# Kernel tuning notes

Measured on AMD Instinct MI355X. Metric: run time of the kernel, lower is better.

The kernel has to match this reference:

```python
import jax, jax.numpy as jnp
import numpy as np

NN_SIZE = 16  # nn_size from __init__


def _knn_idx(points_ref, k):
    """Brute-force KNN of points_ref against itself (replaces faiss_knn).
    Returns (B, N, k) neighbor indices, self point excluded."""
    sq = jnp.sum(points_ref * points_ref, axis=-1)  # (B, N)
    # squared pairwise distances (B, N, N)
    d2 = sq[:, :, None] + sq[:, None, :] - 2.0 * jnp.einsum(
        'bnd,bmd->bnm', points_ref, points_ref)
    _, idx = jax.lax.top_k(-d2, k + 1)  # nearest first; idx[...,0] is self
    return idx[:, :, 1:]


def _edge_lengths(pts, knn_idx):
    """Gather neighbor coords and compute edge lengths (B, N, K)."""
    group = jax.vmap(lambda p, i: p[i])(pts, knn_idx)  # (B, N, K, D)
    return jnp.linalg.norm(group - pts[:, :, None, :], axis=-1)


def setup_inputs() -> dict:
    key = jax.random.key(0)
    k1, k2 = jax.random.split(key)
    B, N, D = 4, 8192, 3
    points_ref = jax.random.normal(k1, (B, N, D), dtype=jnp.float32)
    # pred points: perturbed ref so the loss is non-degenerate
    points = points_ref + 0.01 * jax.random.normal(k2, (B, N, D), dtype=jnp.float32)
    return {"points_ref": points_ref, "points": points}


def reference(points_ref, points):
    # faiss KNN is non-differentiable -> stop_gradient on the index search
    knn_idx = _knn_idx(jax.lax.stop_gradient(points_ref), NN_SIZE)  # (B,N,K)
    dist_ref = _edge_lengths(points_ref, knn_idx)  # (B, N, K)
    dist = _edge_lengths(points, knn_idx)          # (B, N, K)
    # metric = torch.nn.L1Loss() (mean reduction)
    return jnp.mean(jnp.abs(dist_ref - dist))
```

## Files before the change

kernel.cpp:

```cpp
#include <hip/hip_runtime.h>
#include <math.h>

#define BATCH 4
#define NPTS  8192
#define KNN   16
#define KK    17
#define NQ    (BATCH*NPTS)
#define JMASK 0x1FFFu
#define EMASK 0xFFFFE000u
#define TOTAL_EDGES (BATCH*NPTS*KNN)

#define GC    32
#define GLO   (-4.5f)
#define GINV  (32.0f/9.0f)
#define NCELL (GC*GC*GC)

#define NG    128
#define GSZ   64

#define QPB   16
#define BLOCK 256
#define GRIDQ (NQ/QPB)
#define WIN   64
#define CAP   21

__device__ __forceinline__ int cell_coord(float x) {
    int c = (int)floorf((x - GLO) * GINV);
    return min(GC - 1, max(0, c));
}
__device__ __forceinline__ unsigned spread5(unsigned v) {
    v &= 31u;
    v = (v | (v << 8)) & 0x100Fu;
    v = (v | (v << 4)) & 0x10C3u;
    v = (v | (v << 2)) & 0x1249u;
    return v;
}
__device__ __forceinline__ unsigned morton_id(float x, float y, float z) {
    return spread5((unsigned)cell_coord(x)) | (spread5((unsigned)cell_coord(y)) << 1)
         | (spread5((unsigned)cell_coord(z)) << 2);
}
__device__ __forceinline__ unsigned mkkey(const float4 p, float xi, float yi,
                                          float zi, float sqi, unsigned j) {
    const float e  = fmaf(p.x, xi, fmaf(p.y, yi, p.z * zi)) + p.w;
    const float d2 = e + sqi;
    return (__float_as_uint(d2) & EMASK) | j;
}
__device__ __forceinline__ void ins17(unsigned (&a)[KK], unsigned key) {
    #pragma unroll
    for (int k = KK - 1; k >= 1; --k) a[k] = min(a[k], max(a[k - 1], key));
    a[0] = min(a[0], key);
}
template<int RL>
__device__ __forceinline__ unsigned merge_tau(const unsigned (*s_key)[BLOCK], int t) {
    const int mq = t & (QPB - 1), half = (t >> 4) & 1;
    unsigned m[KK];
    #pragma unroll
    for (int k = 0; k < KK; ++k) m[k] = 0xFFFFFFFFu;
    for (int s = 8 * half; s < 8 * half + 8; ++s) {
        const int col = mq + s * QPB;
        for (int k = 0; k < RL; ++k) {
            const unsigned c = s_key[k][col];
            if (c >= m[KK - 1]) break;
            ins17(m, c);
        }
    }
    unsigned tau = 0;
    #pragma unroll
    for (int k = 0; k < KK; ++k) {
        const unsigned bk = (unsigned)__shfl_xor((int)m[KK - 1 - k], 16, 64);
        tau = max(tau, min(m[k], bk));
    }
    return tau;
}

__global__ void pel_hist(const float* __restrict__ pref, unsigned* __restrict__ hist,
                         float* __restrict__ acc, unsigned* __restrict__ bcnt) {
    const int idx = blockIdx.x * 256 + threadIdx.x;
    if (idx == 0) { acc[0] = 0.0f; bcnt[0] = 0u; }
    const int b = idx >> 13;
    const unsigned mid = morton_id(pref[3*idx], pref[3*idx+1], pref[3*idx+2]);
    atomicAdd(&hist[b * NCELL + mid], 1u);
}
__global__ __launch_bounds__(1024)
void pel_scan(const unsigned* __restrict__ hist, unsigned* __restrict__ off) {
    __shared__ unsigned s[1024];
    const unsigned* h = hist + blockIdx.x * NCELL;
    unsigned*       o = off  + blockIdx.x * NCELL;
    const int t = threadIdx.x;
    unsigned v[32], tot = 0;
    #pragma unroll
    for (int k = 0; k < 32; ++k) { v[k] = h[t * 32 + k]; tot += v[k]; }
    s[t] = tot;
    __syncthreads();
    for (int d = 1; d < 1024; d <<= 1) {
        const unsigned add = (t >= d) ? s[t - d] : 0u;
        __syncthreads();
        s[t] += add;
        __syncthreads();
    }
    unsigned run = s[t] - tot;
    #pragma unroll
    for (int k = 0; k < 32; ++k) { o[t * 32 + k] = run; run += v[k]; }
}
__global__ void pel_scatter(const float* __restrict__ pref, const float* __restrict__ pts,
                            unsigned* __restrict__ off,
                            float4* __restrict__ p4r, float4* __restrict__ p4p) {
    const int idx = blockIdx.x * 256 + threadIdx.x;
    const int b = idx >> 13;
    const float x = pref[3*idx], y = pref[3*idx+1], z = pref[3*idx+2];
    const unsigned mid = morton_id(x, y, z);
    const unsigned pos = atomicAdd(&off[b * NCELL + mid], 1u);
    p4r[b * NPTS + pos] = make_float4(-2.f*x, -2.f*y, -2.f*z, fmaf(x, x, fmaf(y, y, z*z)));
    const float px = pts[3*idx], py = pts[3*idx+1], pz = pts[3*idx+2];
    p4p[b * NPTS + pos] = make_float4(-2.f*px, -2.f*py, -2.f*pz,
                                      fmaf(px, px, fmaf(py, py, pz*pz)));
}
__global__ __launch_bounds__(256)
void pel_gstat(const float4* __restrict__ P4r, float4* __restrict__ gball) {
    const int wv = threadIdx.x >> 6, lane = threadIdx.x & 63;
    const int gid = blockIdx.x * 4 + wv;
    const int b = gid >> 7, g = gid & (NG - 1);
    const float4 p = P4r[b * NPTS + g * GSZ + lane];
    const float x = -0.5f * p.x, y = -0.5f * p.y, z = -0.5f * p.z;
    float mnx = x, mxx = x, mny = y, mxy = y, mnz = z, mxz = z;
    #pragma unroll
    for (int m = 1; m <= 32; m <<= 1) {
        mnx = fminf(mnx, __shfl_xor(mnx, m, 64)); mxx = fmaxf(mxx, __shfl_xor(mxx, m, 64));
        mny = fminf(mny, __shfl_xor(mny, m, 64)); mxy = fmaxf(mxy, __shfl_xor(mxy, m, 64));
        mnz = fminf(mnz, __shfl_xor(mnz, m, 64)); mxz = fmaxf(mxz, __shfl_xor(mxz, m, 64));
    }
    const float cx = 0.5f * (mnx + mxx), cy = 0.5f * (mny + mxy), cz = 0.5f * (mnz + mxz);
    float d = sqrtf((x-cx)*(x-cx) + (y-cy)*(y-cy) + (z-cz)*(z-cz));
    #pragma unroll
    for (int m = 1; m <= 32; m <<= 1) d = fmaxf(d, __shfl_xor(d, m, 64));
    if (lane == 0) gball[gid] = make_float4(cx, cy, cz, d);
}

__global__ __launch_bounds__(BLOCK, 8)
void pel_query(const float4* __restrict__ P4r, const float4* __restrict__ P4p,
               const float4* __restrict__ gball,
               float* __restrict__ acc_ws, unsigned* __restrict__ bcnt,
               float* __restrict__ out)
{
    __shared__ unsigned s_key[CAP][BLOCK];
    __shared__ unsigned s_tau[QPB];
    __shared__ unsigned short s_glist[NG];
    __shared__ float s_grp[4];
    __shared__ int s_ng;
    __shared__ float s_part[BLOCK / 64];

    const int t  = threadIdx.x;
    const int lq = t & (QPB - 1), sp = t >> 4;
    const int bid = blockIdx.x;
    const int qg  = ((bid & 7) << 8) | (bid >> 3);
    const int q  = qg * QPB + lq;
    const int b  = q >> 13;
    const int i  = q & (NPTS - 1);

    const float4* __restrict__ Pq = P4r + b * NPTS;
    const float4* __restrict__ Pp = P4p + b * NPTS;
    const float4* __restrict__ Gb = gball + b * NG;

    const float4 self = Pq[i];
    const float xi = -0.5f * self.x, yi = -0.5f * self.y, zi = -0.5f * self.z;
    const float sqi = self.w;

    unsigned al[4] = {~0u, ~0u, ~0u, ~0u};
    const int w0 = min(max(i - WIN / 2, 0), NPTS - WIN) + sp * 4;
    {
        float4 cw[4];
        #pragma unroll
        for (int u = 0; u < 4; ++u) cw[u] = Pq[w0 + u];
        #pragma unroll
        for (int u = 0; u < 4; ++u) {
            const unsigned key = mkkey(cw[u], xi, yi, zi, sqi, (unsigned)(w0 + u));
            #pragma unroll
            for (int k = 3; k >= 1; --k) al[k] = min(al[k], max(al[k - 1], key));
            al[0] = min(al[0], key);
        }
    }
    #pragma unroll
    for (int k = 0; k < 4; ++k) s_key[k][t] = al[k];
    __syncthreads();
    if (t < 32) {
        const unsigned tau0 = merge_tau<4>(s_key, t);
        if (t < QPB) s_tau[t] = tau0;
    }
    __syncthreads();

    if (t < QPB) {
        if (t == 0) s_ng = 0;
        const int i2 = (qg * QPB + t) & (NPTS - 1);
        const float4 s2 = Pq[i2];
        const float qx = -0.5f * s2.x, qy = -0.5f * s2.y, qz = -0.5f * s2.z;
        float mnx = qx, mxx = qx, mny = qy, mxy = qy, mnz = qz, mxz = qz;
        #pragma unroll
        for (int m = 1; m <= 8; m <<= 1) {
            mnx = fminf(mnx, __shfl_xor(mnx, m, 64)); mxx = fmaxf(mxx, __shfl_xor(mxx, m, 64));
            mny = fminf(mny, __shfl_xor(mny, m, 64)); mxy = fmaxf(mxy, __shfl_xor(mxy, m, 64));
            mnz = fminf(mnz, __shfl_xor(mnz, m, 64)); mxz = fmaxf(mxz, __shfl_xor(mxz, m, 64));
        }
        const float cx = 0.5f * (mnx + mxx), cy = 0.5f * (mny + mxy), cz = 0.5f * (mnz + mxz);
        const float dq = sqrtf((qx-cx)*(qx-cx) + (qy-cy)*(qy-cy) + (qz-cz)*(qz-cz));
        const float rt = sqrtf(__uint_as_float((s_tau[t] & EMASK) + 0x2000u));
        float v = dq + rt;
        #pragma unroll
        for (int m = 1; m <= 8; m <<= 1) v = fmaxf(v, __shfl_xor(v, m, 64));
        if (t == 0) {
            s_grp[0] = cx; s_grp[1] = cy; s_grp[2] = cz; s_grp[3] = v + 1e-3f;
        }
    }
    __syncthreads();

    if (t < NG) {
        const float4 gb = Gb[t];
        const float dx = gb.x - s_grp[0], dy = gb.y - s_grp[1], dz = gb.z - s_grp[2];
        const float rhs = s_grp[3] + gb.w;
        if (dx*dx + dy*dy + dz*dz <= rhs * rhs) {
            const int slot = atomicAdd(&s_ng, 1);
            s_glist[slot] = (unsigned short)t;
        }
    }
    __syncthreads();
    const int ng = s_ng;

    unsigned tauL = s_tau[lq];
    int cnt = 0;
    unsigned* skp = &s_key[0][t];
    int gb4n = (int)s_glist[0] * GSZ + sp * 4;
    float4 cn[4];
    #pragma unroll
    for (int u = 0; u < 4; ++u) cn[u] = Pq[gb4n + u];
    for (int gi = 0; gi < ng; ++gi) {
        const int gb4 = gb4n;
        float4 c[4];
        #pragma unroll
        for (int u = 0; u < 4; ++u) c[u] = cn[u];
        const int gin = (gi + 1 < ng) ? gi + 1 : gi;
        gb4n = (int)s_glist[gin] * GSZ + sp * 4;
        #pragma unroll
        for (int u = 0; u < 4; ++u) cn[u] = Pq[gb4n + u];

        #pragma unroll
        for (int u = 0; u < 4; ++u) {
            const unsigned key = mkkey(c[u], xi, yi, zi, sqi, (unsigned)(gb4 + u));
            *skp = key;
            const int a = (key <= tauL) ? 1 : 0;
            skp += a * BLOCK;
            cnt += a;
        }
        if (cnt > CAP - 4) {
            unsigned k17[KK];
            #pragma unroll
            for (int k = 0; k < KK; ++k) k17[k] = 0xFFFFFFFFu;
            for (int n = 0; n < cnt; ++n) ins17(k17, s_key[n][t]);
            const unsigned th = k17[KK - 1];
            int kept = 0;
            for (int n = 0; n < cnt; ++n) {
                const unsigned c2 = s_key[n][t];
                if (c2 <= th) { s_key[kept][t] = c2; ++kept; }
            }
            cnt = kept; tauL = min(tauL, th);
            skp = &s_key[cnt][t];
        }
    }

    unsigned c17[KK];
    #pragma unroll
    for (int k = 0; k < KK; ++k) c17[k] = 0xFFFFFFFFu;
    for (int n = 0; n < cnt; ++n) ins17(c17, s_key[n][t]);
    __syncthreads();
    #pragma unroll
    for (int k = 0; k < KK; ++k) s_key[k][t] = c17[k];
    __syncthreads();
    if (t < 32) {
        const unsigned tauX = merge_tau<KK>(s_key, t);
        if (t < QPB) s_tau[t] = tauX;
    }
    __syncthreads();
    const unsigned tauK = s_tau[lq];

    const float4 selfp = Pp[i];
    const float pxi = -0.5f * selfp.x, pyi = -0.5f * selfp.y, pzi = -0.5f * selfp.z;
    float accv = 0.0f;
    #pragma unroll
    for (int k = 0; k < KK; ++k) {
        if (c17[k] <= tauK) {
            const int j = (int)(c17[k] & JMASK);
            const float4 pr = Pq[j];
            const float er  = fmaf(pr.x, xi, fmaf(pr.y, yi, pr.z * zi)) + pr.w;
            const float d2r = fmaxf(er + sqi, 0.0f);
            const float4 pp = Pp[j];
            const float ep  = fmaf(pp.x, pxi, fmaf(pp.y, pyi, pp.z * pzi)) + pp.w;
            const float d2p = fmaxf(ep + selfp.w, 0.0f);
            accv += fabsf(sqrtf(d2r) - sqrtf(d2p));
        }
    }

    #pragma unroll
    for (int o = 32; o > 0; o >>= 1) accv += __shfl_down(accv, o, 64);
    if ((t & 63) == 0) s_part[t >> 6] = accv;
    __syncthreads();
    if (t == 0) {
        float s = 0.0f;
        #pragma unroll
        for (int w2 = 0; w2 < BLOCK / 64; ++w2) s += s_part[w2];
        atomicAdd(acc_ws, s);
        __threadfence();
        const unsigned old = atomicAdd(bcnt, 1u);
        if (old == GRIDQ - 1) {
            __threadfence();
            const float total = atomicAdd(acc_ws, 0.0f);
            out[0] = total * (1.0f / (float)TOTAL_EDGES);
        }
    }
}

extern "C" void kernel_launch(void* const* d_in, const int* in_sizes, int n_in,
                              void* d_out, int out_size, void* d_ws, size_t ws_size,
                              hipStream_t stream) {
    const float* pref = (const float*)d_in[0];
    const float* pts  = (const float*)d_in[1];
    float4*   P4r  = (float4*)d_ws;
    float4*   P4p  = P4r + NQ;
    unsigned* hist = (unsigned*)d_ws;
    unsigned* off  = (unsigned*)((char*)d_ws + 1048576);
    float4*   gball= (float4*)((char*)d_ws + 1572864);
    float*    acc  = (float*)((char*)d_ws + 1581056);
    unsigned* bcnt = (unsigned*)(acc + 1);
    float*    out  = (float*)d_out;

    hipMemsetAsync(hist, 0, BATCH * NCELL * sizeof(unsigned), stream);
    pel_hist   <<<NQ / 256, 256, 0, stream>>>(pref, hist, acc, bcnt);
    pel_scan   <<<BATCH, 1024, 0, stream>>>(hist, off);
    pel_scatter<<<NQ / 256, 256, 0, stream>>>(pref, pts, off, P4r, P4p);
    pel_gstat  <<<(BATCH * NG) / 4, 256, 0, stream>>>(P4r, gball);
    pel_query  <<<GRIDQ, BLOCK, 0, stream>>>(P4r, P4p, gball, acc, bcnt, out);
}
```

Measured before the change: 259.8 us.

## Shrink KNN query blocks to one wavefront with wave-level merging and ballot culling

Each query block drops from 16 queries and 256 threads to 4 queries and 64 threads, so one block is exactly one wavefront. The single-thread and sub-wave phases (tau merge, query bounding ball, group culling) now run on all lanes using shuffles, ballot and mbcnt compaction, removing shared scratch and several barriers. Each group of 4 queries gets a tighter bounding ball, which should cull more point groups per block. In exchange there are more, smaller blocks and more global atomics in the final reduction, and the launch-bounds occupancy hint is changed.

```diff
diff --git a/kernel.cpp b/kernel.cpp
--- a/kernel.cpp
+++ b/kernel.cpp
@@ -18,8 +18,8 @@
 #define NG    128
 #define GSZ   64
 
-#define QPB   16
-#define BLOCK 256
+#define QPB   4
+#define BLOCK 64
 #define GRIDQ (NQ/QPB)
 #define WIN   64
 #define CAP   21
@@ -50,14 +50,19 @@
     for (int k = KK - 1; k >= 1; --k) a[k] = min(a[k], max(a[k - 1], key));
     a[0] = min(a[0], key);
 }
+__device__ __forceinline__ unsigned mbcnt64(unsigned long long m) {
+    return __builtin_amdgcn_mbcnt_hi((unsigned)(m >> 32),
+           __builtin_amdgcn_mbcnt_lo((unsigned)m, 0u));
+}
 template<int RL>
-__device__ __forceinline__ unsigned merge_tau(const unsigned (*s_key)[BLOCK], int t) {
-    const int mq = t & (QPB - 1), half = (t >> 4) & 1;
+__device__ __forceinline__ unsigned merge_tau4(const unsigned (*s_key)[BLOCK], int t) {
+    const int qb = t & 48;
+    const int h  = (t >> 3) & 1;
     unsigned m[KK];
     #pragma unroll
     for (int k = 0; k < KK; ++k) m[k] = 0xFFFFFFFFu;
-    for (int s = 8 * half; s < 8 * half + 8; ++s) {
-        const int col = mq + s * QPB;
+    for (int s = 8 * h; s < 8 * h + 8; ++s) {
+        const int col = qb + s;
         for (int k = 0; k < RL; ++k) {
             const unsigned c = s_key[k][col];
             if (c >= m[KK - 1]) break;
@@ -67,7 +72,7 @@
     unsigned tau = 0;
     #pragma unroll
     for (int k = 0; k < KK; ++k) {
-        const unsigned bk = (unsigned)__shfl_xor((int)m[KK - 1 - k], 16, 64);
+        const unsigned bk = (unsigned)__shfl_xor((int)m[KK - 1 - k], 8, 64);
         tau = max(tau, min(m[k], bk));
     }
     return tau;
@@ -136,24 +141,21 @@
     if (lane == 0) gball[gid] = make_float4(cx, cy, cz, d);
 }
 
-__global__ __launch_bounds__(BLOCK, 8)
+__global__ __launch_bounds__(BLOCK, 4)
 void pel_query(const float4* __restrict__ P4r, const float4* __restrict__ P4p,
                const float4* __restrict__ gball,
                float* __restrict__ acc_ws, unsigned* __restrict__ bcnt,
                float* __restrict__ out)
 {
     __shared__ unsigned s_key[CAP][BLOCK];
-    __shared__ unsigned s_tau[QPB];
     __shared__ unsigned short s_glist[NG];
-    __shared__ float s_grp[4];
-    __shared__ int s_ng;
-    __shared__ float s_part[BLOCK / 64];
 
     const int t  = threadIdx.x;
-    const int lq = t & (QPB - 1), sp = t >> 4;
+    const int lq = t >> 4;
+    const int sp = t & 15;
     const int bid = blockIdx.x;
-    const int qg  = ((bid & 7) << 8) | (bid >> 3);
-    const int q  = qg * QPB + lq;
+    const int qblk = ((bid & 7) << 10) | (bid >> 3);
+    const int q  = qblk * QPB + lq;
     const int b  = q >> 13;
     const int i  = q & (NPTS - 1);
 
@@ -182,51 +184,43 @@
     #pragma unroll
     for (int k = 0; k < 4; ++k) s_key[k][t] = al[k];
     __syncthreads();
-    if (t < 32) {
-        const unsigned tau0 = merge_tau<4>(s_key, t);
-        if (t < QPB) s_tau[t] = tau0;
-    }
-    __syncthreads();
-
-    if (t < QPB) {
-        if (t == 0) s_ng = 0;
-        const int i2 = (qg * QPB + t) & (NPTS - 1);
-        const float4 s2 = Pq[i2];
-        const float qx = -0.5f * s2.x, qy = -0.5f * s2.y, qz = -0.5f * s2.z;
-        float mnx = qx, mxx = qx, mny = qy, mxy = qy, mnz = qz, mxz = qz;
-        #pragma unroll
-        for (int m = 1; m <= 8; m <<= 1) {
-            mnx = fminf(mnx, __shfl_xor(mnx, m, 64)); mxx = fmaxf(mxx, __shfl_xor(mxx, m, 64));
-            mny = fminf(mny, __shfl_xor(mny, m, 64)); mxy = fmaxf(mxy, __shfl_xor(mxy, m, 64));
-            mnz = fminf(mnz, __shfl_xor(mnz, m, 64)); mxz = fmaxf(mxz, __shfl_xor(mxz, m, 64));
-        }
-        const float cx = 0.5f * (mnx + mxx), cy = 0.5f * (mny + mxy), cz = 0.5f * (mnz + mxz);
-        const float dq = sqrtf((qx-cx)*(qx-cx) + (qy-cy)*(qy-cy) + (qz-cz)*(qz-cz));
-        const float rt = sqrtf(__uint_as_float((s_tau[t] & EMASK) + 0x2000u));
-        float v = dq + rt;
-        #pragma unroll
-        for (int m = 1; m <= 8; m <<= 1) v = fmaxf(v, __shfl_xor(v, m, 64));
-        if (t == 0) {
-            s_grp[0] = cx; s_grp[1] = cy; s_grp[2] = cz; s_grp[3] = v + 1e-3f;
-        }
-    }
-    __syncthreads();
-
-    if (t < NG) {
-        const float4 gb = Gb[t];
-        const float dx = gb.x - s_grp[0], dy = gb.y - s_grp[1], dz = gb.z - s_grp[2];
-        const float rhs = s_grp[3] + gb.w;
-        if (dx*dx + dy*dy + dz*dz <= rhs * rhs) {
-            const int slot = atomicAdd(&s_ng, 1);
-            s_glist[slot] = (unsigned short)t;
-        }
-    }
-    __syncthreads();
-    const int ng = s_ng;
-
-    unsigned tauL = s_tau[lq];
+    const unsigned tau0 = merge_tau4<4>(s_key, t);
+    __syncthreads();
+
+    float mnx = xi, mxx = xi, mny = yi, mxy = yi, mnz = zi, mxz = zi;
+    #pragma unroll
+    for (int m = 16; m <= 32; m <<= 1) {
+        mnx = fminf(mnx, __shfl_xor(mnx, m, 64)); mxx = fmaxf(mxx, __shfl_xor(mxx, m, 64));
+        mny = fminf(mny, __shfl_xor(mny, m, 64)); mxy = fmaxf(mxy, __shfl_xor(mxy, m, 64));
+        mnz = fminf(mnz, __shfl_xor(mnz, m, 64)); mxz = fmaxf(mxz, __shfl_xor(mxz, m, 64));
+    }
+    const float cx = 0.5f * (mnx + mxx), cy = 0.5f * (mny + mxy), cz = 0.5f * (mnz + mxz);
+    const float dq = sqrtf((xi-cx)*(xi-cx) + (yi-cy)*(yi-cy) + (zi-cz)*(zi-cz));
+    const float rt = sqrtf(__uint_as_float((tau0 & EMASK) + 0x2000u));
+    float v = dq + rt;
+    #pragma unroll
+    for (int m = 16; m <= 32; m <<= 1) v = fmaxf(v, __shfl_xor(v, m, 64));
+    const float R   = v + 1e-3f;
+    const float thr = R * R - (cx*cx + cy*cy + cz*cz);
+
+    int ng;
+    {
+        const float4 g1 = Gb[t], g2 = Gb[64 + t];
+        const float d1x = g1.x-cx, d1y = g1.y-cy, d1z = g1.z-cz, r1 = R+g1.w;
+        const float d2x = g2.x-cx, d2y = g2.y-cy, d2z = g2.z-cz, r2 = R+g2.w;
+        const bool h1 = d1x*d1x + d1y*d1y + d1z*d1z <= r1*r1;
+        const bool h2 = d2x*d2x + d2y*d2y + d2z*d2z <= r2*r2;
+        const unsigned long long m1 = __ballot(h1);
+        if (h1) s_glist[mbcnt64(m1)] = (unsigned short)t;
+        const int c1 = (int)__popcll(m1);
+        const unsigned long long m2 = __ballot(h2);
+        if (h2) s_glist[c1 + mbcnt64(m2)] = (unsigned short)(64 + t);
+        ng = c1 + (int)__popcll(m2);
+    }
+    __syncthreads();
+
+    unsigned tauL = tau0;
     int cnt = 0;
-    unsigned* skp = &s_key[0][t];
     int gb4n = (int)s_glist[0] * GSZ + sp * 4;
     float4 cn[4];
     #pragma unroll
@@ -244,10 +238,8 @@
         #pragma unroll
         for (int u = 0; u < 4; ++u) {
             const unsigned key = mkkey(c[u], xi, yi, zi, sqi, (unsigned)(gb4 + u));
-            *skp = key;
-            const int a = (key <= tauL) ? 1 : 0;
-            skp += a * BLOCK;
-            cnt += a;
+            s_key[cnt][t] = key;
+            cnt += (key <= tauL) ? 1 : 0;
         }
         if (cnt > CAP - 4) {
             unsigned k17[KK];
@@ -261,7 +253,6 @@
                 if (c2 <= th) { s_key[kept][t] = c2; ++kept; }
             }
             cnt = kept; tauL = min(tauL, th);
-            skp = &s_key[cnt][t];
         }
     }
 
@@ -273,12 +264,7 @@
     #pragma unroll
     for (int k = 0; k < KK; ++k) s_key[k][t] = c17[k];
     __syncthreads();
-    if (t < 32) {
-        const unsigned tauX = merge_tau<KK>(s_key, t);
-        if (t < QPB) s_tau[t] = tauX;
-    }
-    __syncthreads();
-    const unsigned tauK = s_tau[lq];
+    const unsigned tauK = merge_tau4<KK>(s_key, t);
 
     const float4 selfp = Pp[i];
     const float pxi = -0.5f * selfp.x, pyi = -0.5f * selfp.y, pzi = -0.5f * selfp.z;
@@ -299,13 +285,8 @@
 
     #pragma unroll
     for (int o = 32; o > 0; o >>= 1) accv += __shfl_down(accv, o, 64);
-    if ((t & 63) == 0) s_part[t >> 6] = accv;
-    __syncthreads();
     if (t == 0) {
-        float s = 0.0f;
-        #pragma unroll
-        for (int w2 = 0; w2 < BLOCK / 64; ++w2) s += s_part[w2];
-        atomicAdd(acc_ws, s);
+        atomicAdd(acc_ws, accv);
         __threadfence();
         const unsigned old = atomicAdd(bcnt, 1u);
         if (old == GRIDQ - 1) {
```

New measurement: 416.5 us. 60.3% more time.
